# Kernel optimization log

Measured on AMD Instinct MI355X. Metric: run time of the kernel, lower is better.

The kernel has to match this reference:

```python
import jax, jax.numpy as jnp
import numpy as np
from jax import lax

T_STEPS = 16
TAU = 2.0
ALPHA = 4.0  # sigmoid surrogate sharpness
BN_EPS = 1e-5


def conv1d(x, w, b, stride, pad):
    # x: [N,C,L], w: [O,I,K]
    y = lax.conv_general_dilated(x, w, (stride,), [(pad, pad)],
                                 dimension_numbers=('NCH', 'OIH', 'NCH'))
    return y + b[None, :, None]


def maxpool1d(x):  # kernel 3, stride 2, pad 1 (pad value -inf via init)
    return lax.reduce_window(x, -jnp.inf, lax.max, (1, 1, 3), (1, 1, 2),
                             [(0, 0), (0, 0), (1, 1)])


def spike(x):  # heaviside forward (surrogate only matters for bwd)
    return (x >= 0).astype(x.dtype)


def lif(x_seq):
    # multi-step LIF: v += (x - v)/tau (v_reset=0), spike at v>=1, hard reset, detach_reset
    def step(v, x):
        v = v + (x - v) / TAU
        s = spike(v - 1.0)
        v = v * (1.0 - lax.stop_gradient(s))
        return v, s
    _, s_seq = lax.scan(step, jnp.zeros_like(x_seq[0]), x_seq)
    return s_seq


def seq_apply(f, xs):
    # apply stateless layer over [T,B,...] by folding T into batch
    T, B = xs.shape[0], xs.shape[1]
    y = f(xs.reshape((T * B,) + xs.shape[2:]))
    return y.reshape((T, B) + y.shape[1:])


def setup_inputs() -> dict:
    key = jax.random.key(0)
    ks = jax.random.split(key, 12)
    B, L = 256, 4097
    inp = {
        'x': jax.random.normal(ks[0], (B, L), jnp.float32),
        'conv0_w': jax.random.normal(ks[1], (16, 1, 7), jnp.float32) * 0.2,
        'conv0_b': jax.random.normal(ks[2], (16,), jnp.float32) * 0.1,
        'bn_g': jnp.ones((16,), jnp.float32),
        'bn_b': jnp.zeros((16,), jnp.float32),
        'bn_m': jax.random.normal(ks[3], (16,), jnp.float32) * 0.1,
        'bn_v': jnp.ones((16,), jnp.float32),
        'conv1_w': jax.random.normal(ks[4], (32, 16, 5), jnp.float32) * 0.1,
        'conv1_b': jax.random.normal(ks[5], (32,), jnp.float32) * 0.1,
        'conv2_w': jax.random.normal(ks[6], (64, 32, 3), jnp.float32) * 0.1,
        'conv2_b': jax.random.normal(ks[7], (64,), jnp.float32) * 0.1,
        'fc1_w': jax.random.normal(ks[8], (32, 64), jnp.float32) * 0.12,
        'fc1_b': jax.random.normal(ks[9], (32,), jnp.float32) * 0.1,
        'fc2_w': jax.random.normal(ks[10], (5, 32), jnp.float32) * 0.17,
        'fc2_b': jax.random.normal(ks[11], (5,), jnp.float32) * 0.1,
    }
    return inp


def reference(x, conv0_w, conv0_b, bn_g, bn_b, bn_m, bn_v,
              conv1_w, conv1_b, conv2_w, conv2_b,
              fc1_w, fc1_b, fc2_w, fc2_b):
    # ---- static encoder ----
    h = x[:, None, :]                                  # [B,1,4097]
    h = conv1d(h, conv0_w, conv0_b, 2, 3)              # [B,16,2049]
    h = (h - bn_m[None, :, None]) * lax.rsqrt(bn_v + BN_EPS)[None, :, None] \
        * bn_g[None, :, None] + bn_b[None, :, None]
    h = jax.nn.relu(h)
    h = maxpool1d(h)                                   # [B,16,1025]
    # ---- repeat over T timesteps ----
    hs = jnp.broadcast_to(h[None], (T_STEPS,) + h.shape)  # [T,B,16,1025]
    # ---- spiking trunk ----
    hs = seq_apply(lambda a: conv1d(a, conv1_w, conv1_b, 2, 2), hs)  # [T,B,32,513]
    hs = lif(hs)
    hs = seq_apply(maxpool1d, hs)                      # [T,B,32,257]
    hs = seq_apply(lambda a: conv1d(a, conv2_w, conv2_b, 2, 1), hs)  # [T,B,64,129]
    hs = lif(hs)
    # dropout: identity (inference); adaptive avg pool to 1 + flatten
    hs = hs.mean(axis=-1)                              # [T,B,64]
    # ---- classifier ----
    hs = jnp.einsum('tbd,od->tbo', hs, fc1_w) + fc1_b  # [T,B,32]
    hs = lif(hs)
    hs = jnp.einsum('tbd,od->tbo', hs, fc2_w) + fc2_b  # [T,B,5]
    return hs.mean(axis=0)                             # [B,5]
```

## Files before the change

### kernel.cpp

```cpp
#include <hip/hip_runtime.h>
#include <math.h>


#define NB 256
#define LX 4097
#define LQ 2049
#define LP 1025
#define LJ1 513
#define LP1 257
#define LJ2 129

#define M1S 520
#define S2R 132
#define HSW 260

typedef float f32x4 __attribute__((ext_vector_type(4)));

__global__ __launch_bounds__(256) void kF_front(const float* __restrict__ x,
                                                const float* __restrict__ w0,
                                                const float* __restrict__ b0,
                                                const float* __restrict__ bng,
                                                const float* __restrict__ bnb,
                                                const float* __restrict__ bnm,
                                                const float* __restrict__ bnv,
                                                const float* __restrict__ w1,
                                                const float* __restrict__ b1,
                                                unsigned short* __restrict__ m1,
                                                const float* __restrict__ w2,
                                                float* __restrict__ w2t2) {
  __shared__ __align__(16) float xs[1056];
  __shared__ __align__(16) float hs[16 * HSW];
  __shared__ __align__(16) float wl[2560];
  __shared__ float w0s[112];
  __shared__ float cpar[64];
  __shared__ float rs_l[16];
  int bid = blockIdx.x;
  int b = bid / 5, jt = bid % 5;
  int J0 = jt * 128;
  int Pstart = 2 * J0 - 2;
  int tid = threadIdx.x;

  if (tid < 16) rs_l[tid] = (float)(1.0 / sqrt((double)bnv[tid] + 1e-5));
  {
    const float* xb = x + (size_t)b * LX;
    int xoff = 4 * Pstart - 5;
    for (int i = tid; i < 1056; i += 256) {
      int gi = xoff + i;
      xs[i] = (gi >= 0 && gi < LX) ? xb[gi] : 0.f;
    }
    for (int i = tid; i < 2560; i += 256) {
      int c = i & 31, r = i >> 5;
      wl[i] = w1[c * 80 + r];
    }
    if (tid < 112) w0s[tid] = w0[tid];
    if (tid >= 128 && tid < 192) {
      int i = tid - 128;
      int c = i >> 2, e = i & 3;
      float v = (e == 0) ? bnm[c] : (e == 1) ? bng[c] : (e == 2) ? bnb[c] : b0[c];
      cpar[i] = v;
    }
  }
  __syncthreads();

  {
    int c2 = tid >> 4, g2 = tid & 15;
    float m = cpar[4 * c2], g = cpar[4 * c2 + 1], bb = cpar[4 * c2 + 2],
          bc = cpar[4 * c2 + 3];
    float rs = rs_l[c2];
    float wv[7];
#pragma unroll
    for (int k = 0; k < 7; ++k) wv[k] = w0s[c2 * 7 + k];
    int dp0 = g2 * 17;
    const f32x4* xv = (const f32x4*)xs;
    f32x4 q0 = xv[dp0], q1 = xv[dp0 + 1], q2 = xv[dp0 + 2];
#pragma unroll
    for (int i = 0; i < 17; ++i) {
      int dp = dp0 + i;
      if (dp >= 261) break;
      int p = Pstart + dp;
      float hm = 0.f;
      if (p >= 0 && p < LP) {
        float win[12] = {q0.x, q0.y, q0.z, q0.w, q1.x, q1.y, q1.z, q1.w,
                         q2.x, q2.y, q2.z, q2.w};
        float best = -INFINITY;
#pragma unroll
        for (int dq = -1; dq <= 1; ++dq) {
          int q = 2 * p + dq;
          if (q < 0 || q >= LQ) continue;
          float s = 0.f;
          int base = 2 * dq + 2;
#pragma unroll
          for (int k = 0; k < 7; ++k) s = fmaf(win[base + k], wv[k], s);
          float y = s + bc;
          y = (y - m) * rs * g + bb;
          y = fmaxf(y, 0.f);
          best = fmaxf(best, y);
        }
        hm = best;
      }
      hs[c2 * HSW + dp] = hm;
      q0 = q1; q1 = q2; q2 = xv[dp + 3];
    }
  }
  __syncthreads();

  {
    int c = tid & 31, jg = tid >> 5;
    int jbase = J0 + jg * 16;
    if (jbase <= 512) {
      float acc[16];
#pragma unroll
      for (int i = 0; i < 16; ++i) acc[i] = 0.f;

      for (int ic = 0; ic < 16; ++ic) {
        float win[36];
        const f32x4* row = (const f32x4*)(hs + ic * HSW + 32 * jg);
#pragma unroll
        for (int i = 0; i < 9; ++i) {
          f32x4 v = row[i];
          win[4 * i] = v.x; win[4 * i + 1] = v.y;
          win[4 * i + 2] = v.z; win[4 * i + 3] = v.w;
        }
        float wv[5];
#pragma unroll
        for (int k = 0; k < 5; ++k) wv[k] = wl[(ic * 5 + k) * 32 + c];
#pragma unroll
        for (int j = 0; j < 16; ++j) {
#pragma unroll
          for (int k = 0; k < 5; ++k) acc[j] = fmaf(win[2 * j + k], wv[k], acc[j]);
        }
      }

      float bc = b1[c];
      unsigned mskv[16];
#pragma unroll
      for (int j = 0; j < 16; ++j) {
        float xin = acc[j] + bc;
        float v = 0.f; unsigned mm = 0;
#pragma unroll
        for (int t = 0; t < 16; ++t) {
          v = v + (xin - v) * 0.5f;
          if (v >= 1.f) { mm |= (1u << t); v = 0.f; }
        }
        mskv[j] = mm;
      }
      size_t rowo = ((size_t)b * 32 + c) * M1S + jbase;
      if (jbase + 15 < LJ1) {
        uint4 u0, u1;
        u0.x = mskv[0] | (mskv[1] << 16);
        u0.y = mskv[2] | (mskv[3] << 16);
        u0.z = mskv[4] | (mskv[5] << 16);
        u0.w = mskv[6] | (mskv[7] << 16);
        u1.x = mskv[8] | (mskv[9] << 16);
        u1.y = mskv[10] | (mskv[11] << 16);
        u1.z = mskv[12] | (mskv[13] << 16);
        u1.w = mskv[14] | (mskv[15] << 16);
        *(uint4*)(m1 + rowo) = u0;
        *(uint4*)(m1 + rowo + 8) = u1;
      } else {
        for (int j = 0; j < 16; ++j)
          if (jbase + j < LJ1) m1[rowo + j] = (unsigned short)mskv[j];
      }
    }
  }

  if (bid < 16) {
    for (int idx = bid * 256 + tid; idx < 64 * 32 * 3; idx += 4096) {
      int k = idx % 3; int r = idx / 3; int cc = r % 32; int oc = r / 32;
      w2t2[((size_t)cc * 64 + oc) * 4 + k] = w2[idx];
    }
  }
}

__global__ __launch_bounds__(256) void kD_conv2_lif(const unsigned short* __restrict__ m1,
                                                    const float* __restrict__ w2t2,
                                                    const float* __restrict__ b2,
                                                    unsigned short* __restrict__ s2) {
  __shared__ __align__(16) float F[288 * 20];
  __shared__ unsigned mval[288];
  __shared__ unsigned short mbuf[32 * 20];
  int bid = blockIdx.x;
  int b = bid / 33, jt = bid % 33;
  int j0 = jt * 4;
  int tid = threadIdx.x;
  int w = tid >> 6;
  int lane = tid & 63;

  const unsigned short* m1b = m1 + (size_t)b * 32 * M1S;
  int qbase = 4 * j0 - 3;
  for (int i = tid; i < 1024; i += 256) {
    int c = i >> 5, u = i & 31;
    if (u < 20) {
      int q = qbase + u;
      mbuf[c * 20 + u] = (q >= 0 && q <= 512) ? m1b[(size_t)c * M1S + q] : (unsigned short)0;
    }
  }
  __syncthreads();

  for (int it = tid; it < 288; it += 256) {
    int c = it / 9, idx = it - c * 9;
    int p = 2 * j0 - 1 + idx;
    unsigned m = 0;
    if (p >= 0 && p < LP1) {
      const unsigned short* mr = mbuf + c * 20;
      int l0 = 2 * idx;
      m = (unsigned)mr[l0] | (unsigned)mr[l0 + 1] | (unsigned)mr[l0 + 2];
    }
    mval[it] = m;
    f32x4* Fr = (f32x4*)(F + it * 20);
    f32x4 f0, f1, f2, f3;
    f0.x = (float)(m & 1u);         f0.y = (float)((m >> 1) & 1u);
    f0.z = (float)((m >> 2) & 1u);  f0.w = (float)((m >> 3) & 1u);
    f1.x = (float)((m >> 4) & 1u);  f1.y = (float)((m >> 5) & 1u);
    f1.z = (float)((m >> 6) & 1u);  f1.w = (float)((m >> 7) & 1u);
    f2.x = (float)((m >> 8) & 1u);  f2.y = (float)((m >> 9) & 1u);
    f2.z = (float)((m >> 10) & 1u); f2.w = (float)((m >> 11) & 1u);
    f3.x = (float)((m >> 12) & 1u); f3.y = (float)((m >> 13) & 1u);
    f3.z = (float)((m >> 14) & 1u); f3.w = (float)((m >> 15) & 1u);
    Fr[0] = f0; Fr[1] = f1; Fr[2] = f2; Fr[3] = f3;
  }
  __syncthreads();

  unsigned bits;
  {
    bool nz = false;
    if (lane < 32) {
      int base9 = lane * 9 + 2 * w;
      nz = (mval[base9] | mval[base9 + 1] | mval[base9 + 2]) != 0u;
    }
    bits = (unsigned)__ballot(nz);
  }

  float acc[16];
#pragma unroll
  for (int t = 0; t < 16; ++t) acc[t] = 0.f;

  const f32x4* wbase = (const f32x4*)w2t2 + lane;
  while (bits) {
    int c = __builtin_ctz(bits);
    bits &= bits - 1;
    int base9 = c * 9 + 2 * w;
    unsigned mv0 = mval[base9];
    unsigned mv1 = mval[base9 + 1];
    unsigned mv2 = mval[base9 + 2];
    f32x4 wq = wbase[c * 64];
    const float* Fb = F + base9 * 20;
    if (mv0) {
      const f32x4* Fp = (const f32x4*)Fb;
      f32x4 fv[4];
      fv[0] = Fp[0]; fv[1] = Fp[1]; fv[2] = Fp[2]; fv[3] = Fp[3];
#pragma unroll
      for (int t = 0; t < 16; ++t) acc[t] = fmaf(wq.x, fv[t >> 2][t & 3], acc[t]);
    }
    if (mv1) {
      const f32x4* Fp = (const f32x4*)(Fb + 20);
      f32x4 fv[4];
      fv[0] = Fp[0]; fv[1] = Fp[1]; fv[2] = Fp[2]; fv[3] = Fp[3];
#pragma unroll
      for (int t = 0; t < 16; ++t) acc[t] = fmaf(wq.y, fv[t >> 2][t & 3], acc[t]);
    }
    if (mv2) {
      const f32x4* Fp = (const f32x4*)(Fb + 40);
      f32x4 fv[4];
      fv[0] = Fp[0]; fv[1] = Fp[1]; fv[2] = Fp[2]; fv[3] = Fp[3];
#pragma unroll
      for (int t = 0; t < 16; ++t) acc[t] = fmaf(wq.z, fv[t >> 2][t & 3], acc[t]);
    }
  }

  int j = j0 + w;
  if (j < LJ2) {
    float bc = b2[lane];
    float v = 0.f; unsigned mm = 0;
#pragma unroll
    for (int t = 0; t < 16; ++t) {
      float xin = acc[t] + bc;
      v = v + (xin - v) * 0.5f;
      if (v >= 1.f) { mm |= (1u << t); v = 0.f; }
    }
    s2[((size_t)b * S2R + j) * 64 + lane] = (unsigned short)mm;
  }
}

__global__ __launch_bounds__(256) void kE_head(const unsigned short* __restrict__ s2,
                                               const float* __restrict__ fc1w,
                                               const float* __restrict__ fc1b,
                                               const float* __restrict__ fc2w,
                                               const float* __restrict__ fc2b,
                                               float* __restrict__ out) {
  __shared__ unsigned cntL[4][16][64];
  __shared__ float meanL[16][64];
  __shared__ unsigned s3m[32];
  int b = blockIdx.x;
  int tid = threadIdx.x;
  int w = tid >> 6, lane = tid & 63;

  int j0 = (w == 0) ? 0 : 33 + 32 * (w - 1);
  int jc = (w == 0) ? 33 : 32;
  const unsigned short* base = s2 + (size_t)b * S2R * 64 + lane;
  unsigned cnt[16];
#pragma unroll
  for (int t = 0; t < 16; ++t) cnt[t] = 0;
  for (int u = 0; u < jc; ++u) {
    unsigned m = base[(size_t)(j0 + u) * 64];
#pragma unroll
    for (int t = 0; t < 16; ++t) cnt[t] += (m >> t) & 1u;
  }
#pragma unroll
  for (int t = 0; t < 16; ++t) cntL[w][t][lane] = cnt[t];
  __syncthreads();

#pragma unroll
  for (int i = 0; i < 4; ++i) {
    int idx = tid + 256 * i;
    int t = idx >> 6, oc = idx & 63;
    unsigned s = cntL[0][t][oc] + cntL[1][t][oc] + cntL[2][t][oc] + cntL[3][t][oc];
    meanL[t][oc] = (float)s / 129.f;
  }
  __syncthreads();

  if (tid < 32) {
    int o = tid;
    const float* wrow = fc1w + o * 64;
    float bb = fc1b[o];
    float v = 0.f;
    unsigned msk = 0;
    for (int t = 0; t < 16; ++t) {
      float s = 0.f;
      for (int d = 0; d < 64; ++d) s = fmaf(meanL[t][d], wrow[d], s);
      float xin = s + bb;
      v = v + (xin - v) * 0.5f;
      if (v >= 1.f) { msk |= (1u << t); v = 0.f; }
    }
    s3m[o] = msk;
  }
  __syncthreads();

  if (tid < 5) {
    int q = tid;
    const float* wrow = fc2w + q * 32;
    float bb = fc2b[q];
    float accs = 0.f;
    for (int t = 0; t < 16; ++t) {
      float s = 0.f;
      for (int o = 0; o < 32; ++o) s += (((s3m[o] >> t) & 1u) ? wrow[o] : 0.f);
      accs += (s + bb);
    }
    out[b * 5 + q] = accs / 16.f;
  }
}

extern "C" void kernel_launch(void* const* d_in, const int* in_sizes, int n_in,
                              void* d_out, int out_size, void* d_ws, size_t ws_size,
                              hipStream_t stream) {
  const float* x   = (const float*)d_in[0];
  const float* w0  = (const float*)d_in[1];
  const float* b0  = (const float*)d_in[2];
  const float* bng = (const float*)d_in[3];
  const float* bnb = (const float*)d_in[4];
  const float* bnm = (const float*)d_in[5];
  const float* bnv = (const float*)d_in[6];
  const float* w1  = (const float*)d_in[7];
  const float* b1  = (const float*)d_in[8];
  const float* w2  = (const float*)d_in[9];
  const float* b2  = (const float*)d_in[10];
  const float* f1w = (const float*)d_in[11];
  const float* f1b = (const float*)d_in[12];
  const float* f2w = (const float*)d_in[13];
  const float* f2b = (const float*)d_in[14];
  float* out = (float*)d_out;

  char* ws = (char*)d_ws;
  size_t sz_m1 = (size_t)NB * 32 * M1S * 2;
  size_t sz_s2 = (size_t)NB * S2R * 64 * 2;
  size_t off_s2 = sz_m1;
  size_t off_w2 = off_s2 + sz_s2;
  if (ws_size < off_w2 + 32768) return;

  unsigned short* m1 = (unsigned short*)ws;
  unsigned short* s2 = (unsigned short*)(ws + off_s2);
  float* w2t2 = (float*)(ws + off_w2);

  kF_front<<<NB * 5, 256, 0, stream>>>(x, w0, b0, bng, bnb, bnm, bnv, w1, b1, m1, w2, w2t2);
  kD_conv2_lif<<<NB * 33, 256, 0, stream>>>(m1, w2t2, b2, s2);
  kE_head<<<NB, 256, 0, stream>>>(s2, f1w, f1b, f2w, f2b, out);
}
```

Measured before the change: 112.2 us.

## Replace LIF recurrence with threshold-count lookup and retile front kernel

Measured after the change: 161.8 us. 44.2% more time.

```diff
diff --git a/kernel.cpp b/kernel.cpp
--- a/kernel.cpp
+++ b/kernel.cpp
@@ -12,9 +12,45 @@
 
 #define M1S 520
 #define S2R 132
-#define HSW 260
+#define JT 96
+#define HSW 196
+#define XSN 792
 
 typedef float f32x4 __attribute__((ext_vector_type(4)));
+
+__global__ __launch_bounds__(256) void kT_setup(const float* __restrict__ w2,
+                                                float* __restrict__ w2t2,
+                                                float* __restrict__ thr_g,
+                                                unsigned* __restrict__ mtab_g) {
+  int tid = threadIdx.x;
+  for (int idx = tid; idx < 64 * 32 * 3; idx += 256) {
+    int k = idx % 3; int r = idx / 3; int cc = r % 32; int oc = r / 32;
+    w2t2[((size_t)cc * 64 + oc) * 4 + k] = w2[idx];
+  }
+  if (tid < 16) {
+    int p = tid + 1;
+    unsigned lo = __float_as_uint(1.0f), hi = __float_as_uint(2.0f);
+    while (hi - lo > 1u) {
+      unsigned mid = lo + (hi - lo) / 2u;
+      float x = __uint_as_float(mid);
+      float v = 0.f; bool sp = false;
+      for (int s = 0; s < p; ++s) {
+        v = v + (x - v) * 0.5f;
+        if (v >= 1.f) { sp = true; break; }
+      }
+      if (sp) hi = mid; else lo = mid;
+    }
+    thr_g[tid] = __uint_as_float(hi);
+  }
+  if (tid < 17) {
+    unsigned mask = 0;
+    if (tid >= 1) {
+      int p = 17 - tid;
+      for (int t = p - 1; t < 16; t += p) mask |= (1u << t);
+    }
+    mtab_g[tid] = mask;
+  }
+}
 
 __global__ __launch_bounds__(256) void kF_front(const float* __restrict__ x,
                                                 const float* __restrict__ w0,
@@ -26,25 +62,27 @@
                                                 const float* __restrict__ w1,
                                                 const float* __restrict__ b1,
                                                 unsigned short* __restrict__ m1,
-                                                const float* __restrict__ w2,
-                                                float* __restrict__ w2t2) {
-  __shared__ __align__(16) float xs[1056];
+                                                const float* __restrict__ thr_g,
+                                                const unsigned* __restrict__ mtab_g) {
+  __shared__ __align__(16) float xs[XSN];
   __shared__ __align__(16) float hs[16 * HSW];
   __shared__ __align__(16) float wl[2560];
   __shared__ float w0s[112];
   __shared__ float cpar[64];
   __shared__ float rs_l[16];
+  __shared__ unsigned mtab_s[17];
   int bid = blockIdx.x;
-  int b = bid / 5, jt = bid % 5;
-  int J0 = jt * 128;
+  int b = bid / 6, jt = bid % 6;
+  int J0 = jt * JT;
   int Pstart = 2 * J0 - 2;
   int tid = threadIdx.x;
 
   if (tid < 16) rs_l[tid] = (float)(1.0 / sqrt((double)bnv[tid] + 1e-5));
+  if (tid < 17) mtab_s[tid] = mtab_g[tid];
   {
     const float* xb = x + (size_t)b * LX;
     int xoff = 4 * Pstart - 5;
-    for (int i = tid; i < 1056; i += 256) {
+    for (int i = tid; i < XSN; i += 256) {
       int gi = xoff + i;
       xs[i] = (gi >= 0 && gi < LX) ? xb[gi] : 0.f;
     }
@@ -60,6 +98,9 @@
       cpar[i] = v;
     }
   }
+  float thrv[16];
+#pragma unroll
+  for (int i = 0; i < 16; ++i) thrv[i] = thr_g[i];
   __syncthreads();
 
   {
@@ -70,13 +111,13 @@
     float wv[7];
 #pragma unroll
     for (int k = 0; k < 7; ++k) wv[k] = w0s[c2 * 7 + k];
-    int dp0 = g2 * 17;
+    int dp0 = g2 * 13;
     const f32x4* xv = (const f32x4*)xs;
     f32x4 q0 = xv[dp0], q1 = xv[dp0 + 1], q2 = xv[dp0 + 2];
 #pragma unroll
-    for (int i = 0; i < 17; ++i) {
+    for (int i = 0; i < 13; ++i) {
       int dp = dp0 + i;
-      if (dp >= 261) break;
+      if (dp >= 195) break;
       int p = Pstart + dp;
       float hm = 0.f;
       if (p >= 0 && p < LP) {
@@ -106,17 +147,17 @@
 
   {
     int c = tid & 31, jg = tid >> 5;
-    int jbase = J0 + jg * 16;
+    int jbase = J0 + jg * 12;
     if (jbase <= 512) {
-      float acc[16];
-#pragma unroll
-      for (int i = 0; i < 16; ++i) acc[i] = 0.f;
+      float acc[12];
+#pragma unroll
+      for (int i = 0; i < 12; ++i) acc[i] = 0.f;
 
       for (int ic = 0; ic < 16; ++ic) {
-        float win[36];
-        const f32x4* row = (const f32x4*)(hs + ic * HSW + 32 * jg);
-#pragma unroll
-        for (int i = 0; i < 9; ++i) {
+        float win[28];
+        const f32x4* row = (const f32x4*)(hs + ic * HSW + 24 * jg);
+#pragma unroll
+        for (int i = 0; i < 7; ++i) {
           f32x4 v = row[i];
           win[4 * i] = v.x; win[4 * i + 1] = v.y;
           win[4 * i + 2] = v.z; win[4 * i + 3] = v.w;
@@ -125,49 +166,35 @@
 #pragma unroll
         for (int k = 0; k < 5; ++k) wv[k] = wl[(ic * 5 + k) * 32 + c];
 #pragma unroll
-        for (int j = 0; j < 16; ++j) {
+        for (int j = 0; j < 12; ++j) {
 #pragma unroll
           for (int k = 0; k < 5; ++k) acc[j] = fmaf(win[2 * j + k], wv[k], acc[j]);
         }
       }
 
       float bc = b1[c];
-      unsigned mskv[16];
-#pragma unroll
-      for (int j = 0; j < 16; ++j) {
+      unsigned mskv[12];
+#pragma unroll
+      for (int j = 0; j < 12; ++j) {
         float xin = acc[j] + bc;
-        float v = 0.f; unsigned mm = 0;
-#pragma unroll
-        for (int t = 0; t < 16; ++t) {
-          v = v + (xin - v) * 0.5f;
-          if (v >= 1.f) { mm |= (1u << t); v = 0.f; }
-        }
-        mskv[j] = mm;
+        int cnt = 0;
+#pragma unroll
+        for (int i = 0; i < 16; ++i) cnt += (xin >= thrv[i]) ? 1 : 0;
+        mskv[j] = mtab_s[cnt];
       }
       size_t rowo = ((size_t)b * 32 + c) * M1S + jbase;
-      if (jbase + 15 < LJ1) {
-        uint4 u0, u1;
-        u0.x = mskv[0] | (mskv[1] << 16);
-        u0.y = mskv[2] | (mskv[3] << 16);
-        u0.z = mskv[4] | (mskv[5] << 16);
-        u0.w = mskv[6] | (mskv[7] << 16);
-        u1.x = mskv[8] | (mskv[9] << 16);
-        u1.y = mskv[10] | (mskv[11] << 16);
-        u1.z = mskv[12] | (mskv[13] << 16);
-        u1.w = mskv[14] | (mskv[15] << 16);
-        *(uint4*)(m1 + rowo) = u0;
-        *(uint4*)(m1 + rowo + 8) = u1;
+      if (jbase + 11 < LJ1) {
+        uint2 u0, u1, u2;
+        u0.x = mskv[0] | (mskv[1] << 16);  u0.y = mskv[2] | (mskv[3] << 16);
+        u1.x = mskv[4] | (mskv[5] << 16);  u1.y = mskv[6] | (mskv[7] << 16);
+        u2.x = mskv[8] | (mskv[9] << 16);  u2.y = mskv[10] | (mskv[11] << 16);
+        *(uint2*)(m1 + rowo) = u0;
+        *(uint2*)(m1 + rowo + 4) = u1;
+        *(uint2*)(m1 + rowo + 8) = u2;
       } else {
-        for (int j = 0; j < 16; ++j)
+        for (int j = 0; j < 12; ++j)
           if (jbase + j < LJ1) m1[rowo + j] = (unsigned short)mskv[j];
       }
-    }
-  }
-
-  if (bid < 16) {
-    for (int idx = bid * 256 + tid; idx < 64 * 32 * 3; idx += 4096) {
-      int k = idx % 3; int r = idx / 3; int cc = r % 32; int oc = r / 32;
-      w2t2[((size_t)cc * 64 + oc) * 4 + k] = w2[idx];
     }
   }
 }
@@ -375,13 +402,17 @@
   size_t sz_s2 = (size_t)NB * S2R * 64 * 2;
   size_t off_s2 = sz_m1;
   size_t off_w2 = off_s2 + sz_s2;
-  if (ws_size < off_w2 + 32768) return;
+  size_t off_th = off_w2 + 32768;
+  if (ws_size < off_th + 256) return;
 
   unsigned short* m1 = (unsigned short*)ws;
   unsigned short* s2 = (unsigned short*)(ws + off_s2);
   float* w2t2 = (float*)(ws + off_w2);
-
-  kF_front<<<NB * 5, 256, 0, stream>>>(x, w0, b0, bng, bnb, bnm, bnv, w1, b1, m1, w2, w2t2);
+  float* thr_g = (float*)(ws + off_th);
+  unsigned* mtab_g = (unsigned*)(ws + off_th + 64);
+
+  kT_setup<<<1, 256, 0, stream>>>(w2, w2t2, thr_g, mtab_g);
+  kF_front<<<NB * 6, 256, 0, stream>>>(x, w0, b0, bng, bnb, bnm, bnv, w1, b1, m1, thr_g, mtab_g);
   kD_conv2_lif<<<NB * 33, 256, 0, stream>>>(m1, w2t2, b2, s2);
   kE_head<<<NB, 256, 0, stream>>>(s2, f1w, f1b, f2w, f2b, out);
 }
```
